# Kernel tuning notes

Measured on AMD Instinct MI355X. Metric: run time of the kernel, lower is better.

Reference implementation:

```python
import jax, jax.numpy as jnp
import numpy as np

K_SIGN = 100000.0   # tanh sharpness approximating sign()
EPS = 1e-05         # acos clamp epsilon


def setup_inputs() -> dict:
    key = jax.random.key(0)
    B, N, KV = 2, 8, 64
    contour = jax.random.uniform(key, (B, N, KV, 2), dtype=jnp.float32)  # values in [0,1]
    return {"contour": contour, "size": 128}


def reference(contour, size):
    b, n, kv, _ = contour.shape
    dt = contour.dtype
    # pixel grid, normalized by size (matches torch meshgrid 'ij' + reshape(-1,2)/size)
    g = jnp.arange(size, dtype=dt)
    mesh = jnp.stack(jnp.meshgrid(g, g, indexing="ij"), axis=-1).reshape(-1, 2) / size  # (S2, 2)

    c = contour.reshape(b * n, 1, kv, 2)          # (bn, 1, kv, 2)
    diff = c - mesh[None, :, None, :]             # (bn, S2, kv, 2)
    roll_diff = jnp.roll(diff, -1, axis=2)        # next vertex

    # sign = diff * swap(roll_diff); sign[...,1]-sign[...,0] = d_y*rd_x - d_x*rd_y
    cross = diff[..., 1] * roll_diff[..., 0] - diff[..., 0] * roll_diff[..., 1]
    sign = jnp.tanh(K_SIGN * cross)               # (bn, S2, kv)

    norm_diff = jnp.linalg.norm(diff, axis=3)
    norm_roll = jnp.linalg.norm(roll_diff, axis=3)
    scalar = jnp.sum(diff * roll_diff, axis=3)
    cosang = jnp.clip(scalar / (norm_diff * norm_roll), -1.0 + EPS, 1.0 - EPS)
    angles = jnp.arccos(cosang)                   # (bn, S2, kv)

    sum_angles = jnp.clip(jnp.abs(jnp.sum(sign * angles, axis=2) / (2.0 * jnp.pi)), 0.0, 1.0)
    return sum_angles.reshape(b, n, size, size)
```

## Files before the change

### kernel.cpp

```cpp
#include <hip/hip_runtime.h>
#include <math.h>

#define BLOCK 256
#define SPLIT 4
#define PPT   2
#define MAX_KV_LDS 1024

typedef float v2f __attribute__((ext_vector_type(2)));

__device__ __forceinline__ float rcp1(float x) { return __builtin_amdgcn_rcpf(x); }

__device__ __forceinline__ v2f edge_term(v2f cross, v2f dot)
{
    v2f t = cross * 100000.0f;
    v2f s = t * t;
    v2f pn = (s + 105.0f) * s + 945.0f;
    v2f num = t * pn;
    v2f qd = (15.0f * s + 420.0f) * s + 945.0f;
    v2f th;
    th.x = __builtin_amdgcn_fmed3f(num.x * rcp1(qd.x), -1.0f, 1.0f);
    th.y = __builtin_amdgcn_fmed3f(num.y * rcp1(qd.y), -1.0f, 1.0f);

    v2f ac = { fabsf(cross.x), fabsf(cross.y) };
    v2f ad = { fabsf(dot.x),   fabsf(dot.y)   };
    v2f mn = { fminf(ac.x, ad.x), fminf(ac.y, ad.y) };
    v2f mx = { fmaxf(ac.x, ad.x), fmaxf(ac.y, ad.y) };
    v2f a  = { mn.x * rcp1(mx.x), mn.y * rcp1(mx.y) };
    v2f s2 = a * a;
    v2f r = 0.0208351f * s2 - 0.0851330f;
    r = r * s2 + 0.1801410f;
    r = r * s2 - 0.3302995f;
    r = r * s2 + 0.9998660f;
    r = r * a;
    v2f rhi = 1.57079632679f - r;
    r.x = (ac.x > ad.x) ? rhi.x : r.x;
    r.y = (ac.y > ad.y) ? rhi.y : r.y;
    v2f rneg = 3.14159265359f - r;
    r.x = (dot.x < 0.0f) ? rneg.x : r.x;
    r.y = (dot.y < 0.0f) ? rneg.y : r.y;

    return th * r;
}

__device__ __forceinline__ v2f winding_pk(const float2* __restrict__ verts,
                                          int k0, int k1, v2f mx2, v2f my2)
{
    v2f acc = {0.0f, 0.0f};
    if (k0 >= k1) return acc;
    float2 v = verts[k0];
    v2f dx = v.x - mx2, dy = v.y - my2;

    #pragma unroll 4
    for (int k = k0; k < k1; ++k) {
        float2 vn = verts[k + 1];
        v2f rx = vn.x - mx2, ry = vn.y - my2;
        v2f cross = dy * rx - dx * ry;
        v2f dot   = dx * rx + dy * ry;
        acc = acc + edge_term(cross, dot);
        dx = rx; dy = ry;
    }
    return acc;
}

__device__ __forceinline__ float winding_scalar(const float2* __restrict__ vsrc,
                                                int kv, int k0, int k1,
                                                float mxs, float mys)
{
    float acc = 0.0f;
    if (k0 >= k1) return acc;
    float2 v = vsrc[k0];
    float dx = v.x - mxs, dy = v.y - mys;
    for (int k = k0; k < k1; ++k) {
        int kn = k + 1; if (kn == kv) kn = 0;
        float2 vn = vsrc[kn];
        float rx = vn.x - mxs, ry = vn.y - mys;
        v2f cross = { dy * rx - dx * ry, 0.0f };
        v2f dot   = { fmaf(dx, rx, dy * ry), 1.0f };
        acc += edge_term(cross, dot).x;
        dx = rx; dy = ry;
    }
    return acc;
}

__global__ __launch_bounds__(BLOCK)
void contour_mask_kernel(const float2* __restrict__ contour,
                         const int* __restrict__ size_ptr,
                         float* __restrict__ out,
                         int out_size, int in0_elems)
{
    __shared__ float2 verts[MAX_KV_LDS + 1];

    const int size     = *size_ptr;
    const int S2       = size * size;
    const int bn_total = out_size / S2;
    const int kv       = in0_elems / (bn_total * 2);

    const int tid  = threadIdx.x;
    const int PIX_PER_BLOCK = (BLOCK / SPLIT) * PPT;
    const int base = blockIdx.x * PIX_PER_BLOCK;

    const int bn0 = base / S2;
    const int rem = base - bn0 * S2;
    const bool one_image = (rem + PIX_PER_BLOCK <= S2) &&
                           (base + PIX_PER_BLOCK <= out_size);
    const bool use_lds = (kv <= MAX_KV_LDS) && one_image;

    if (use_lds) {
        for (int i = tid; i < kv; i += BLOCK)
            verts[i] = contour[(size_t)bn0 * kv + i];
        if (tid == 0)
            verts[kv] = contour[(size_t)bn0 * kv];
    }
    __syncthreads();

    const int seg = tid & (SPLIT - 1);
    const int q   = (kv + SPLIT - 1) / SPLIT;
    const int k0  = min(seg * q, kv);
    const int k1  = min(k0 + q, kv);
    const float inv_size = 1.0f / (float)size;
    const float INV2PI = 0.15915494309189535f;

    if (use_lds) {
        const int pi0 = rem / size;
        const int pj0 = rem - pi0 * size;
        const int t   = (tid / SPLIT) * PPT;

        int pjA = pj0 + t, piA = pi0;
        while (pjA >= size) { pjA -= size; ++piA; }
        int pjB = pjA + 1, piB = piA;
        if (pjB >= size) { pjB = 0; ++piB; }

        v2f mx2 = { piA * inv_size, piB * inv_size };
        v2f my2 = { pjA * inv_size, pjB * inv_size };

        v2f acc = winding_pk(verts, k0, k1, mx2, my2);
        acc.x += __shfl_xor(acc.x, 1, 64);
        acc.y += __shfl_xor(acc.y, 1, 64);
        acc.x += __shfl_xor(acc.x, 2, 64);
        acc.y += __shfl_xor(acc.y, 2, 64);

        if (seg == 0) {
            float2 res;
            res.x = fminf(fabsf(acc.x) * INV2PI, 1.0f);
            res.y = fminf(fabsf(acc.y) * INV2PI, 1.0f);
            *(float2*)(out + base + t) = res;
        }
    } else {
        #pragma unroll
        for (int px = 0; px < PPT; ++px) {
            const int pixel = base + (tid / SPLIT) * PPT + px;
            float a = 0.0f;
            if (pixel < out_size) {
                const int bn = pixel / S2;
                const int p  = pixel - bn * S2;
                const int pi = p / size;
                const int pj = p - pi * size;
                a = winding_scalar(contour + (size_t)bn * kv, kv, k0, k1,
                                   pi * inv_size, pj * inv_size);
            }
            a += __shfl_xor(a, 1, 64);
            a += __shfl_xor(a, 2, 64);
            if (pixel < out_size && seg == 0)
                out[pixel] = fminf(fabsf(a) * INV2PI, 1.0f);
        }
    }
}

extern "C" void kernel_launch(void* const* d_in, const int* in_sizes, int n_in,
                              void* d_out, int out_size, void* d_ws, size_t ws_size,
                              hipStream_t stream)
{
    const float2* contour  = (const float2*)d_in[0];
    const int*    size_ptr = (const int*)d_in[1];
    float*        out      = (float*)d_out;

    const int PIX_PER_BLOCK = (BLOCK / SPLIT) * PPT;
    const int blocks = (out_size + PIX_PER_BLOCK - 1) / PIX_PER_BLOCK;
    contour_mask_kernel<<<blocks, BLOCK, 0, stream>>>(
        contour, size_ptr, out, out_size, in_sizes[0]);
}
```

Baseline: 68.41 us.

## Use rsqrt-based acos, fully unroll fixed kv=64 path, share x terms across pixel pair

Replaces the atan2-style angle polynomial (min/max, reciprocal, select chains) with an acos approximation built from cos = dot*rsqrt(cross^2+dot^2) plus sqrt(1-y)*poly. It adds a specialized fast path for kv==64 with even size that fully unrolls 16 edges per thread and shares the x-difference products between the two adjacent pixels. It also adds an occupancy hint to launch_bounds and drops the packed-float2 vector code. The acos polynomial has different accuracy characteristics, and the fast path is specialized to the test's kv.

```diff
diff --git a/kernel.cpp b/kernel.cpp
--- a/kernel.cpp
+++ b/kernel.cpp
@@ -6,83 +6,29 @@
 #define PPT   2
 #define MAX_KV_LDS 1024
 
-typedef float v2f __attribute__((ext_vector_type(2)));
+__device__ __forceinline__ float rcp1(float x)  { return __builtin_amdgcn_rcpf(x); }
+__device__ __forceinline__ float rsq1(float x)  { return __builtin_amdgcn_rsqf(x); }
+__device__ __forceinline__ float sqrt1(float x) { return __builtin_amdgcn_sqrtf(x); }
 
-__device__ __forceinline__ float rcp1(float x) { return __builtin_amdgcn_rcpf(x); }
-
-__device__ __forceinline__ v2f edge_term(v2f cross, v2f dot)
+__device__ __forceinline__ float edge_term_s(float cr, float dt)
 {
-    v2f t = cross * 100000.0f;
-    v2f s = t * t;
-    v2f pn = (s + 105.0f) * s + 945.0f;
-    v2f num = t * pn;
-    v2f qd = (15.0f * s + 420.0f) * s + 945.0f;
-    v2f th;
-    th.x = __builtin_amdgcn_fmed3f(num.x * rcp1(qd.x), -1.0f, 1.0f);
-    th.y = __builtin_amdgcn_fmed3f(num.y * rcp1(qd.y), -1.0f, 1.0f);
-
-    v2f ac = { fabsf(cross.x), fabsf(cross.y) };
-    v2f ad = { fabsf(dot.x),   fabsf(dot.y)   };
-    v2f mn = { fminf(ac.x, ad.x), fminf(ac.y, ad.y) };
-    v2f mx = { fmaxf(ac.x, ad.x), fmaxf(ac.y, ad.y) };
-    v2f a  = { mn.x * rcp1(mx.x), mn.y * rcp1(mx.y) };
-    v2f s2 = a * a;
-    v2f r = 0.0208351f * s2 - 0.0851330f;
-    r = r * s2 + 0.1801410f;
-    r = r * s2 - 0.3302995f;
-    r = r * s2 + 0.9998660f;
-    r = r * a;
-    v2f rhi = 1.57079632679f - r;
-    r.x = (ac.x > ad.x) ? rhi.x : r.x;
-    r.y = (ac.y > ad.y) ? rhi.y : r.y;
-    v2f rneg = 3.14159265359f - r;
-    r.x = (dot.x < 0.0f) ? rneg.x : r.x;
-    r.y = (dot.y < 0.0f) ? rneg.y : r.y;
-
-    return th * r;
+    float n2 = fmaf(cr, cr, dt * dt);
+    float co = dt * rsq1(n2);
+    co = __builtin_amdgcn_fmed3f(co, -0.99999f, 0.99999f);
+    float y = fabsf(co);
+    float p = fmaf(fmaf(fmaf(-0.0187293f, y, 0.0742610f), y, -0.2121144f),
+                   y, 1.5707288f);
+    float a = sqrt1(1.0f - y) * p;
+    a = (co >= 0.0f) ? a : (3.14159265358979f - a);
+    float t  = cr * 100000.0f;
+    float s  = t * t;
+    float nm = t * fmaf(s + 105.0f, s, 945.0f);
+    float qd = fmaf(fmaf(15.0f, s, 420.0f), s, 945.0f);
+    float th = __builtin_amdgcn_fmed3f(nm * rcp1(qd), -1.0f, 1.0f);
+    return th * a;
 }
 
-__device__ __forceinline__ v2f winding_pk(const float2* __restrict__ verts,
-                                          int k0, int k1, v2f mx2, v2f my2)
-{
-    v2f acc = {0.0f, 0.0f};
-    if (k0 >= k1) return acc;
-    float2 v = verts[k0];
-    v2f dx = v.x - mx2, dy = v.y - my2;
-
-    #pragma unroll 4
-    for (int k = k0; k < k1; ++k) {
-        float2 vn = verts[k + 1];
-        v2f rx = vn.x - mx2, ry = vn.y - my2;
-        v2f cross = dy * rx - dx * ry;
-        v2f dot   = dx * rx + dy * ry;
-        acc = acc + edge_term(cross, dot);
-        dx = rx; dy = ry;
-    }
-    return acc;
-}
-
-__device__ __forceinline__ float winding_scalar(const float2* __restrict__ vsrc,
-                                                int kv, int k0, int k1,
-                                                float mxs, float mys)
-{
-    float acc = 0.0f;
-    if (k0 >= k1) return acc;
-    float2 v = vsrc[k0];
-    float dx = v.x - mxs, dy = v.y - mys;
-    for (int k = k0; k < k1; ++k) {
-        int kn = k + 1; if (kn == kv) kn = 0;
-        float2 vn = vsrc[kn];
-        float rx = vn.x - mxs, ry = vn.y - mys;
-        v2f cross = { dy * rx - dx * ry, 0.0f };
-        v2f dot   = { fmaf(dx, rx, dy * ry), 1.0f };
-        acc += edge_term(cross, dot).x;
-        dx = rx; dy = ry;
-    }
-    return acc;
-}
-
-__global__ __launch_bounds__(BLOCK)
+__global__ __launch_bounds__(BLOCK, 8)
 void contour_mask_kernel(const float2* __restrict__ contour,
                          const int* __restrict__ size_ptr,
                          float* __restrict__ out,
@@ -114,55 +60,89 @@
     __syncthreads();
 
     const int seg = tid & (SPLIT - 1);
-    const int q   = (kv + SPLIT - 1) / SPLIT;
-    const int k0  = min(seg * q, kv);
-    const int k1  = min(k0 + q, kv);
     const float inv_size = 1.0f / (float)size;
     const float INV2PI = 0.15915494309189535f;
 
-    if (use_lds) {
+    if (use_lds && kv == 64 && (size & 1) == 0) {
         const int pi0 = rem / size;
         const int pj0 = rem - pi0 * size;
         const int t   = (tid / SPLIT) * PPT;
 
         int pjA = pj0 + t, piA = pi0;
         while (pjA >= size) { pjA -= size; ++piA; }
-        int pjB = pjA + 1, piB = piA;
-        if (pjB >= size) { pjB = 0; ++piB; }
 
-        v2f mx2 = { piA * inv_size, piB * inv_size };
-        v2f my2 = { pjA * inv_size, pjB * inv_size };
+        const float mx  = (float)piA * inv_size;
+        const float myA = (float)pjA * inv_size;
 
-        v2f acc = winding_pk(verts, k0, k1, mx2, my2);
-        acc.x += __shfl_xor(acc.x, 1, 64);
-        acc.y += __shfl_xor(acc.y, 1, 64);
-        acc.x += __shfl_xor(acc.x, 2, 64);
-        acc.y += __shfl_xor(acc.y, 2, 64);
+        const int k0 = seg * 16;
+        float2 v = verts[k0];
+        float dx  = v.x - mx;
+        float dyA = v.y - myA;
+        float dyB = dyA - inv_size;
+        float accA = 0.0f, accB = 0.0f;
+
+        #pragma unroll
+        for (int k = 0; k < 16; ++k) {
+            float2 vn = verts[k0 + k + 1];
+            float rx  = vn.x - mx;
+            float ryA = vn.y - myA;
+            float ryB = ryA - inv_size;
+            float P   = dx * rx;
+            float dtA = fmaf(dyA, ryA, P);
+            float dtB = fmaf(dyB, ryB, P);
+            float crA = fmaf(dyA, rx, -(dx * ryA));
+            float crB = fmaf(dyB, rx, -(dx * ryB));
+            accA += edge_term_s(crA, dtA);
+            accB += edge_term_s(crB, dtB);
+            dx = rx; dyA = ryA; dyB = ryB;
+        }
+
+        accA += __shfl_xor(accA, 1, 64);
+        accB += __shfl_xor(accB, 1, 64);
+        accA += __shfl_xor(accA, 2, 64);
+        accB += __shfl_xor(accB, 2, 64);
 
         if (seg == 0) {
             float2 res;
-            res.x = fminf(fabsf(acc.x) * INV2PI, 1.0f);
-            res.y = fminf(fabsf(acc.y) * INV2PI, 1.0f);
+            res.x = fminf(fabsf(accA) * INV2PI, 1.0f);
+            res.y = fminf(fabsf(accB) * INV2PI, 1.0f);
             *(float2*)(out + base + t) = res;
         }
-    } else {
-        #pragma unroll
-        for (int px = 0; px < PPT; ++px) {
-            const int pixel = base + (tid / SPLIT) * PPT + px;
-            float a = 0.0f;
-            if (pixel < out_size) {
-                const int bn = pixel / S2;
-                const int p  = pixel - bn * S2;
-                const int pi = p / size;
-                const int pj = p - pi * size;
-                a = winding_scalar(contour + (size_t)bn * kv, kv, k0, k1,
-                                   pi * inv_size, pj * inv_size);
+        return;
+    }
+
+    const int q  = (kv + SPLIT - 1) / SPLIT;
+    const int k0 = min(seg * q, kv);
+    const int k1 = min(k0 + q, kv);
+
+    #pragma unroll
+    for (int px = 0; px < PPT; ++px) {
+        const int pixel = base + (tid / SPLIT) * PPT + px;
+        float a = 0.0f;
+        if (pixel < out_size && k0 < k1) {
+            const int bn = pixel / S2;
+            const int p  = pixel - bn * S2;
+            const int pi = p / size;
+            const int pj = p - pi * size;
+            const float mxs = pi * inv_size;
+            const float mys = pj * inv_size;
+            const float2* vsrc = contour + (size_t)bn * kv;
+            float2 v = vsrc[k0];
+            float dx = v.x - mxs, dy = v.y - mys;
+            for (int k = k0; k < k1; ++k) {
+                int kn = k + 1; if (kn == kv) kn = 0;
+                float2 vn = vsrc[kn];
+                float rx = vn.x - mxs, ry = vn.y - mys;
+                float cr = fmaf(dy, rx, -(dx * ry));
+                float dt = fmaf(dx, rx, dy * ry);
+                a += edge_term_s(cr, dt);
+                dx = rx; dy = ry;
             }
-            a += __shfl_xor(a, 1, 64);
-            a += __shfl_xor(a, 2, 64);
-            if (pixel < out_size && seg == 0)
-                out[pixel] = fminf(fabsf(a) * INV2PI, 1.0f);
         }
+        a += __shfl_xor(a, 1, 64);
+        a += __shfl_xor(a, 2, 64);
+        if (pixel < out_size && seg == 0)
+            out[pixel] = fminf(fabsf(a) * INV2PI, 1.0f);
     }
 }
 
```

New measurement: 69.52 us. No clear change (+1.6%).
